# Kernel optimization log

Measured on AMD Instinct MI355X. Metric: run time of the kernel, lower is better.

Reference implementation:

```python
import jax, jax.numpy as jnp
import numpy as np
import math

B, N, DIM = 2, 2048, 1024
D_LAYERS, H, DH = 6, 8, 64
INNER = H * DH            # 512
FF_IN = int(DIM * 2 * 4 / 3)  # 2730 (GEGLU inner dim)
NB, MD = 32, 128          # rel-pos buckets / max distance
ALPHA = 0.1               # grad_shrink alpha
EPS = 1e-5


def setup_inputs() -> dict:
    key = jax.random.key(0)
    ks = jax.random.split(key, 8)
    s = 0.02
    return {
        "x": jax.random.normal(ks[0], (B, N, DIM), jnp.float32),
        "rel_emb": jax.random.normal(ks[1], (NB, H), jnp.float32) * s,
        "ln1_g": jnp.ones((D_LAYERS, DIM), jnp.float32),
        "ln1_b": jnp.zeros((D_LAYERS, DIM), jnp.float32),
        "wq": jax.random.normal(ks[2], (D_LAYERS, DIM, INNER), jnp.float32) * s,
        "wkv": jax.random.normal(ks[3], (D_LAYERS, DIM, 2 * DH), jnp.float32) * s,
        "wo": jax.random.normal(ks[4], (D_LAYERS, INNER, DIM), jnp.float32) * s,
        "ln2_g": jnp.ones((D_LAYERS, DIM), jnp.float32),
        "ln2_b": jnp.zeros((D_LAYERS, DIM), jnp.float32),
        "w1": jax.random.normal(ks[5], (D_LAYERS, DIM, 2 * FF_IN), jnp.float32) * s,
        "w2": jax.random.normal(ks[6], (D_LAYERS, FF_IN, DIM), jnp.float32) * s,
        "lnf_g": jnp.ones((DIM,), jnp.float32),
        "lnf_b": jnp.zeros((DIM,), jnp.float32),
    }


def _ln(x, g, b):
    mu = jnp.mean(x, axis=-1, keepdims=True)
    var = jnp.mean(jnp.square(x - mu), axis=-1, keepdims=True)
    return (x - mu) * jax.lax.rsqrt(var + EPS) * g + b


def _rel_pos_bias(rel_emb, n):
    pos = jnp.arange(n)
    rel = pos[None, :] - pos[:, None]        # k_pos - q_pos
    dist = jnp.maximum(-rel, 0)
    max_exact = NB // 2
    is_small = dist < max_exact
    val_large = max_exact + (
        jnp.log(jnp.maximum(dist, 1).astype(jnp.float32) / max_exact)
        / math.log(MD / max_exact) * (NB - max_exact)
    ).astype(jnp.int32)
    val_large = jnp.minimum(val_large, NB - 1)
    bucket = jnp.where(is_small, dist, val_large)
    return jnp.transpose(rel_emb[bucket], (2, 0, 1))  # [H, n, n]


def reference(x, rel_emb, ln1_g, ln1_b, wq, wkv, wo, ln2_g, ln2_b, w1, w2, lnf_g, lnf_b):
    b, n, _ = x.shape
    scale = DH ** -0.5
    # grad_shrink (forward identity, scales gradient by alpha)
    x = x * ALPHA + jax.lax.stop_gradient(x) * (1.0 - ALPHA)
    bias = _rel_pos_bias(rel_emb, n)               # [H, n, n]
    causal = jnp.triu(jnp.ones((n, n), bool), 1)   # mask above diagonal
    neg = -jnp.finfo(x.dtype).max
    for l in range(D_LAYERS):
        # --- causal self-attention (multi-query: shared k/v) ---
        xn = _ln(x, ln1_g[l], ln1_b[l])
        q = (xn @ wq[l]).reshape(b, n, H, DH).transpose(0, 2, 1, 3) * scale  # bhnd
        k, v = jnp.split(xn @ wkv[l], 2, axis=-1)                            # [b,n,DH] each
        sim = jnp.einsum('bhid,bjd->bhij', q, k) + bias[None]
        sim = jnp.where(causal, neg, sim)
        attn = jax.nn.softmax(sim, axis=-1)
        o = jnp.einsum('bhij,bjd->bhid', attn, v).transpose(0, 2, 1, 3).reshape(b, n, INNER)
        x = x + o @ wo[l]
        # --- GEGLU feedforward ---
        xn = _ln(x, ln2_g[l], ln2_b[l])
        h = xn @ w1[l]
        a, g = jnp.split(h, 2, axis=-1)
        x = x + (jax.nn.gelu(g, approximate=False) * a) @ w2[l]
    return _ln(x, lnf_g, lnf_b)
```

## Files before the change

kernel.cpp:

```cpp
#include <hip/hip_runtime.h>
#include <cstdint>
#include <cstddef>

using bf16 = __bf16;
typedef __bf16 bf16x8 __attribute__((ext_vector_type(8)));
typedef __bf16 bf16x4 __attribute__((ext_vector_type(4)));
typedef __bf16 bf16x2 __attribute__((ext_vector_type(2)));
typedef float  f32x4  __attribute__((ext_vector_type(4)));
typedef float  f32x16 __attribute__((ext_vector_type(16)));
typedef int    i32x4  __attribute__((ext_vector_type(4)));
typedef float  f32x4u __attribute__((ext_vector_type(4), aligned(4)));

constexpr int NB   = 2;
constexpr int NN   = 2048;
constexpr int DIM  = 1024;
constexpr int NH   = 8;
constexpr int DH   = 64;
constexpr int INNER= 512;
constexpr int QKVN = 640;
constexpr int FF   = 2730;
constexpr int FFP  = 2816;
constexpr int FF2N = 5632;
constexpr int MROW = NB * NN;
constexpr int NLAY = 6;
constexpr int AROWS = NB * NH * NN;
constexpr int NSPLIT = 4;

__device__ __forceinline__ void gload_lds16(const bf16* g, bf16* l) {
  __builtin_amdgcn_global_load_lds((const __attribute__((address_space(1))) void*)g,
                                   (__attribute__((address_space(3))) void*)l,
                                   16, 0, 0);
}

__device__ __forceinline__ int pack_bf16(float lo, float hi_) {
  bf16x2 t; t[0] = (bf16)lo; t[1] = (bf16)hi_;
  return __builtin_bit_cast(int, t);
}

__global__ void btab_kernel(const float* __restrict__ rel, float* __restrict__ btab) {
  int d = blockIdx.x * 256 + threadIdx.x;
  if (d >= NN) return;
  int bucket;
  if (d < 16) bucket = d;
  else {
    int vl = 16 + (int)(logf((float)d / 16.0f) / logf(8.0f) * 16.0f);
    bucket = vl < 31 ? vl : 31;
  }
  for (int h = 0; h < NH; ++h) btab[h * NN + d] = rel[bucket * NH + h];
}

__global__ void conv_tr(const float* __restrict__ src, size_t srcLayer, int srcStride,
                        int colOff, int R, int C,
                        bf16* __restrict__ dst, size_t dstLayer, int Tcols, float scale) {
  __shared__ float tile[32][33];
  const int i0 = blockIdx.x * 32, j0 = blockIdx.y * 32, z = blockIdx.z;
  const float* s = src + (size_t)z * srcLayer;
  bf16* d = dst + (size_t)z * dstLayer;
  const int tx = threadIdx.x, ty = threadIdx.y;
#pragma unroll
  for (int k = 0; k < 4; ++k) {
    int j = j0 + ty + k * 8;
    int i = i0 + tx;
    float v = 0.0f;
    if (j < R && i < C) v = s[(size_t)j * srcStride + colOff + i] * scale;
    tile[ty + k * 8][tx] = v;
  }
  __syncthreads();
#pragma unroll
  for (int k = 0; k < 4; ++k) {
    int i = i0 + ty + k * 8;
    int j = j0 + tx;
    d[(size_t)i * Tcols + j] = (bf16)tile[tx][ty + k * 8];
  }
}

template <typename OUT>
__global__ void ln_kernel(const float* __restrict__ X, const float* __restrict__ G,
                          const float* __restrict__ Bt, OUT* __restrict__ out) {
  __shared__ float red[8];
  const int row = blockIdx.x, t = threadIdx.x;
  const float* xr = X + (size_t)row * DIM;
  float4 v = *(const float4*)(xr + t * 4);
  float s  = v.x + v.y + v.z + v.w;
  float s2 = v.x * v.x + v.y * v.y + v.z * v.z + v.w * v.w;
#pragma unroll
  for (int o = 1; o < 64; o <<= 1) { s += __shfl_xor(s, o); s2 += __shfl_xor(s2, o); }
  if ((t & 63) == 0) { red[t >> 6] = s; red[4 + (t >> 6)] = s2; }
  __syncthreads();
  float S  = red[0] + red[1] + red[2] + red[3];
  float S2 = red[4] + red[5] + red[6] + red[7];
  const float inv = 1.0f / (float)DIM;
  float mu = S * inv;
  float var = S2 * inv - mu * mu;
  float rstd = rsqrtf(var + 1e-5f);
  float4 g  = *(const float4*)(G + t * 4);
  float4 bb = *(const float4*)(Bt + t * 4);
  OUT* orow = out + (size_t)row * DIM + t * 4;
  orow[0] = (OUT)((v.x - mu) * rstd * g.x + bb.x);
  orow[1] = (OUT)((v.y - mu) * rstd * g.y + bb.y);
  orow[2] = (OUT)((v.z - mu) * rstd * g.z + bb.z);
  orow[3] = (OUT)((v.w - mu) * rstd * g.w + bb.w);
}

template <int MODE>
__launch_bounds__(512)
__global__ void gemm_bt(const bf16* __restrict__ A, const bf16* __restrict__ B,
                        int K, int lda, int N, bf16* __restrict__ Cb, float* __restrict__ Xr) {
  __shared__ __align__(16) bf16 As[2][128 * 64];
  __shared__ __align__(16) bf16 Bs[2][128 * 64];
  const int tid = threadIdx.x;
  const int lane = tid & 63, wave = tid >> 6;
  const int gx = gridDim.x, gy = gridDim.y;
  const int nwg = gx * gy;
  const int orig = blockIdx.y * gx + blockIdx.x;
  const int wgid = (orig & 7) * (nwg >> 3) + (orig >> 3);
  const int m0 = (wgid % gy) * 128;
  const int n0 = (wgid / gy) * 128;
  const int wm = (wave >> 2) * 64, wn = (wave & 3) * 32;
  const int fr = lane & 15, fg8 = (lane >> 4) * 8;
  const int frl8 = (fr & 7) * 8;
  const int rL = lane >> 3;
  const int cS = ((lane & 7) ^ rL) * 8;
  const bf16* aB = A + (size_t)(m0 + wave * 8 + rL) * lda + cS;
  const bf16* bB = B + (size_t)(n0 + wave * 8 + rL) * K + cS;
  f32x4 acc[4][2] = {};

  auto STAGE = [&](int buf, int kt) {
#pragma unroll
    for (int r = 0; r < 2; ++r) {
      gload_lds16(aB + (size_t)(r * 64) * lda + kt, &As[buf][(r * 8 + wave) * 512]);
      gload_lds16(bB + (size_t)(r * 64) * K + kt, &Bs[buf][(r * 8 + wave) * 512]);
    }
  };

  STAGE(0, 0);
  const int nt = K >> 6;
  int cur = 0;
  for (int t = 0; t < nt; ++t) {
    asm volatile("s_waitcnt vmcnt(0)" ::: "memory");
    __builtin_amdgcn_s_barrier();
    __builtin_amdgcn_sched_barrier(0);
    if (t + 1 < nt) STAGE(cur ^ 1, (t + 1) * 64);
#pragma unroll
    for (int kk = 0; kk < 64; kk += 32) {
      bf16x8 af[4], bfr[2];
#pragma unroll
      for (int m = 0; m < 4; ++m)
        af[m] = *(const bf16x8*)&As[cur][(wm + m * 16 + fr) * 64 + ((kk + fg8) ^ frl8)];
#pragma unroll
      for (int n = 0; n < 2; ++n)
        bfr[n] = *(const bf16x8*)&Bs[cur][(wn + n * 16 + fr) * 64 + ((kk + fg8) ^ frl8)];
#pragma unroll
      for (int m = 0; m < 4; ++m)
#pragma unroll
        for (int n = 0; n < 2; ++n)
          acc[m][n] = __builtin_amdgcn_mfma_f32_16x16x32_bf16(af[m], bfr[n], acc[m][n], 0, 0, 0);
    }
    __builtin_amdgcn_sched_barrier(0);
    __builtin_amdgcn_s_barrier();
    cur ^= 1;
  }
  const int cc = lane & 15, cg = (lane >> 4) * 4;
#pragma unroll
  for (int m = 0; m < 4; ++m) {
#pragma unroll
    for (int n = 0; n < 2; ++n) {
      const int col = n0 + wn + n * 16 + cc;
#pragma unroll
      for (int r = 0; r < 4; ++r) {
        const int row = m0 + wm + m * 16 + cg + r;
        const size_t idx = (size_t)row * N + col;
        if (MODE == 0) Cb[idx] = (bf16)acc[m][n][r];
        else           Xr[idx] += acc[m][n][r];
      }
    }
  }
}

__global__ void vt_kernel(const bf16* __restrict__ QKV, bf16* __restrict__ VT) {
  __shared__ bf16 t[32][33];
  const int n0 = blockIdx.x * 32, d0 = blockIdx.y * 32, b = blockIdx.z;
  const int tx = threadIdx.x, ty = threadIdx.y;
#pragma unroll
  for (int k = 0; k < 4; ++k) {
    int n = n0 + ty + k * 8;
    t[ty + k * 8][tx] = QKV[(size_t)(b * NN + n) * QKVN + 576 + d0 + tx];
  }
  __syncthreads();
#pragma unroll
  for (int k = 0; k < 4; ++k) {
    int dh = d0 + ty + k * 8;
    VT[(size_t)(b * 64 + dh) * NN + n0 + tx] = t[tx][ty + k * 8];
  }
}

__launch_bounds__(256)
__global__ void attn_kernel(const bf16* __restrict__ QKV, const bf16* __restrict__ VT,
                            const float* __restrict__ btab,
                            float* __restrict__ Opart, float* __restrict__ mlbuf) {
  const int tid = threadIdx.x;
  const int lane = tid & 63, wv = tid >> 6;
  const int split = blockIdx.x & (NSPLIT - 1);
  const int qt = (NN / 32 - 1) - (blockIdx.x / NSPLIT);
  const int h = blockIdx.y * 4 + wv, b = blockIdx.z;
  const int q0 = qt * 32;
  const int qc = lane & 31;
  const int hid = lane >> 5;
  const int h8 = hid * 8;
  const int kv_full = q0 + 32;
  const int nt32 = kv_full >> 5;
  const int base = nt32 >> 2, rem = nt32 & 3;
  const int cnt = base + (split < rem ? 1 : 0);
  const int startT = split * base + (split < rem ? split : rem);
  const int lo = startT * 32;
  const int kend = lo + cnt * 32;
  const size_t obase = ((size_t)split * NB * NH + b * NH + h) * 64;
  const int Rbase = (b * NH + h) * NN + q0;
  if (cnt == 0) {
#pragma unroll
    for (int dd = 0; dd < 32; ++dd)
      Opart[(obase + dd * 2 + hid) * NN + q0 + qc] = 0.0f;
    if (hid == 0)
      ((float2*)mlbuf)[(size_t)split * AROWS + Rbase + qc] = make_float2(-1e30f, 0.0f);
    return;
  }
  const float* bt = btab + h * NN;
  bf16x8 qf[4];
#pragma unroll
  for (int ks = 0; ks < 4; ++ks)
    qf[ks] = *(const bf16x8*)&QKV[(size_t)(b * NN + q0 + qc) * QKVN + h * DH + ks * 16 + h8];

  f32x16 Oacc0 = {}, Oacc1 = {};
  float m_run = -1e30f, l_run = 0.0f;
  int kv0 = lo;

  while (kv0 < kend) {
    const bool interior = (kv0 + 32 <= q0);
    bf16x8 kf[4];
#pragma unroll
    for (int ks = 0; ks < 4; ++ks)
      kf[ks] = *(const bf16x8*)&QKV[(size_t)(b * NN + kv0 + qc) * QKVN + 512 + ks * 16 + h8];
    bf16x8 vf[2][2];
#pragma unroll
    for (int dblk = 0; dblk < 2; ++dblk)
#pragma unroll
      for (int ks2 = 0; ks2 < 2; ++ks2)
        vf[dblk][ks2] = *(const bf16x8*)&VT[(size_t)(b * 64 + dblk * 32 + qc) * NN + kv0 + ks2 * 16 + h8];
    __builtin_amdgcn_s_setprio(1);
    f32x16 S = {};
#pragma unroll
    for (int ks = 0; ks < 4; ++ks)
      S = __builtin_amdgcn_mfma_f32_32x32x16_bf16(kf[ks], qf[ks], S, 0, 0, 0);
    __builtin_amdgcn_s_setprio(0);
    float sv[16];
    float mx = -1e30f;
    if (interior) {
      f32x4 bv[4];
#pragma unroll
      for (int g = 0; g < 4; ++g)
        bv[g] = *(const f32x4u*)(bt + (q0 + qc - kv0 - 8 * g - 4 * hid - 3));
#pragma unroll
      for (int g = 0; g < 4; ++g)
#pragma unroll
        for (int e = 0; e < 4; ++e) {
          const float val = S[g * 4 + e] + bv[g][3 - e];
          sv[g * 4 + e] = val;
          mx = fmaxf(mx, val);
        }
    } else {
#pragma unroll
      for (int r = 0; r < 16; ++r) {
        const int kvr = (r & 3) + 8 * (r >> 2) + 4 * hid;
        const int d = (q0 + qc) - (kv0 + kvr);
        const int dc = d > 0 ? d : 0;
        float val = S[r] + bt[dc];
        if (d < 0) val = -1e30f;
        sv[r] = val;
        mx = fmaxf(mx, val);
      }
    }
    if (!__all(mx <= m_run + 8.0f)) {
      mx = fmaxf(mx, __shfl_xor(mx, 32));
      const float m_new = fmaxf(m_run, mx);
      const float sc = __expf(m_run - m_new);
      l_run *= sc;
#pragma unroll
      for (int r = 0; r < 16; ++r) { Oacc0[r] *= sc; Oacc1[r] *= sc; }
      m_run = m_new;
    }
    float csum = 0.0f;
#pragma unroll
    for (int r = 0; r < 16; ++r) { sv[r] = __expf(sv[r] - m_run); csum += sv[r]; }
    csum += __shfl_xor(csum, 32);
    l_run += csum;
    int w[8];
#pragma unroll
    for (int g = 0; g < 4; ++g) {
      w[2 * g]     = pack_bf16(sv[4 * g],     sv[4 * g + 1]);
      w[2 * g + 1] = pack_bf16(sv[4 * g + 2], sv[4 * g + 3]);
    }
    bf16x8 pfrag[2];
#pragma unroll
    for (int ks2 = 0; ks2 < 2; ++ks2) {
      const int a  = w[4 * ks2],     bb = w[4 * ks2 + 1];
      const int c  = w[4 * ks2 + 2], dd = w[4 * ks2 + 3];
      const int s0 = hid ? a : c,    s1 = hid ? bb : dd;
      const int r0 = __shfl_xor(s0, 32);
      const int r1 = __shfl_xor(s1, 32);
      i32x4 fw;
      fw[0] = hid ? r0 : a;
      fw[1] = hid ? r1 : bb;
      fw[2] = hid ? c  : r0;
      fw[3] = hid ? dd : r1;
      pfrag[ks2] = __builtin_bit_cast(bf16x8, fw);
    }
    __builtin_amdgcn_s_setprio(1);
#pragma unroll
    for (int ks2 = 0; ks2 < 2; ++ks2) {
      Oacc0 = __builtin_amdgcn_mfma_f32_32x32x16_bf16(vf[0][ks2], pfrag[ks2], Oacc0, 0, 0, 0);
      Oacc1 = __builtin_amdgcn_mfma_f32_32x32x16_bf16(vf[1][ks2], pfrag[ks2], Oacc1, 0, 0, 0);
    }
    __builtin_amdgcn_s_setprio(0);
    kv0 += 32;
  }
#pragma unroll
  for (int r = 0; r < 16; ++r) {
    const int dl = (r & 3) + 8 * (r >> 2) + 4 * hid;
    Opart[(obase + dl) * NN + q0 + qc]      = Oacc0[r];
    Opart[(obase + 32 + dl) * NN + q0 + qc] = Oacc1[r];
  }
  if (hid == 0)
    ((float2*)mlbuf)[(size_t)split * AROWS + Rbase + qc] = make_float2(m_run, l_run);
}

__global__ void attn_combine(const float* __restrict__ Opart, const float* __restrict__ mlbuf,
                             bf16* __restrict__ O) {
  const int gtid = blockIdx.x * 256 + threadIdx.x;
  const int q  = gtid & (NN - 1);
  const int dq = (gtid >> 11) & 15;
  const int bh = gtid >> 15;
  const int R = bh * NN + q;
  float2 ml[NSPLIT];
  float m = -1e30f;
#pragma unroll
  for (int s = 0; s < NSPLIT; ++s) {
    ml[s] = ((const float2*)mlbuf)[(size_t)s * AROWS + R];
    m = fmaxf(m, ml[s].x);
  }
  float w[NSPLIT];
  float denom = 0.0f;
#pragma unroll
  for (int s = 0; s < NSPLIT; ++s) {
    w[s] = __expf(ml[s].x - m);
    denom += ml[s].y * w[s];
  }
  const float inv = 1.0f / denom;
  float o[4] = {};
#pragma unroll
  for (int s = 0; s < NSPLIT; ++s) {
    const size_t rbase = ((size_t)(s * NB * NH + bh) * 64 + dq * 4) * NN + q;
#pragma unroll
    for (int j = 0; j < 4; ++j) o[j] += Opart[rbase + j * NN] * w[s];
  }
  bf16x4 res;
#pragma unroll
  for (int j = 0; j < 4; ++j) res[j] = (bf16)(o[j] * inv);
  const int h = bh & (NH - 1), b = bh >> 3;
  *(bf16x4*)&O[(size_t)(b * NN + q) * INNER + h * DH + dq * 4] = res;
}

__global__ void gelu_mul_kernel(bf16* __restrict__ h) {
  const size_t total = (size_t)MROW * FFP / 8;
  for (size_t i = (size_t)blockIdx.x * blockDim.x + threadIdx.x; i < total;
       i += (size_t)gridDim.x * blockDim.x) {
    const size_t row = i / (FFP / 8), c8 = i % (FFP / 8);
    bf16* base = h + row * FF2N + c8 * 8;
    bf16x8 a = *(const bf16x8*)base;
    bf16x8 g = *(const bf16x8*)(base + FFP);
    bf16x8 r;
#pragma unroll
    for (int j = 0; j < 8; ++j) {
      float gv = (float)g[j], av = (float)a[j];
      float ge = 0.5f * gv * (1.0f + erff(gv * 0.70710678118654752f));
      r[j] = (bf16)(ge * av);
    }
    *(bf16x8*)base = r;
  }
}

extern "C" void kernel_launch(void* const* d_in, const int* in_sizes, int n_in,
                              void* d_out, int out_size, void* d_ws, size_t ws_size,
                              hipStream_t stream) {
  (void)in_sizes; (void)n_in; (void)out_size;
  const float* in_x  = (const float*)d_in[0];
  const float* rel   = (const float*)d_in[1];
  const float* ln1g  = (const float*)d_in[2];
  const float* ln1b  = (const float*)d_in[3];
  const float* wq    = (const float*)d_in[4];
  const float* wkv   = (const float*)d_in[5];
  const float* wo    = (const float*)d_in[6];
  const float* ln2g  = (const float*)d_in[7];
  const float* ln2b  = (const float*)d_in[8];
  const float* w1    = (const float*)d_in[9];
  const float* w2    = (const float*)d_in[10];
  const float* lnfg  = (const float*)d_in[11];
  const float* lnfb  = (const float*)d_in[12];
  float* out = (float*)d_out;

  constexpr size_t E_QKV = (size_t)QKVN * DIM;
  constexpr size_t E_WO  = (size_t)DIM * INNER;
  constexpr size_t E_W1F = (size_t)FF2N * DIM;
  constexpr size_t E_W2  = (size_t)DIM * FFP;
  bf16* wqkvT = (bf16*)d_ws;
  bf16* woT  = wqkvT + NLAY * E_QKV;
  bf16* w1fT = woT  + NLAY * E_WO;
  bf16* w2T  = w1fT + NLAY * E_W1F;
  bf16* xnb  = w2T  + NLAY * E_W2;
  bf16* qkvb = xnb  + (size_t)MROW * DIM;
  bf16* vTb  = qkvb + (size_t)MROW * QKVN;
  bf16* ob   = vTb  + (size_t)NB * 64 * NN;
  bf16* hb   = ob   + (size_t)MROW * INNER;
  float* xbuf = (float*)(hb + (size_t)MROW * FF2N);
  float* btab = xbuf + (size_t)MROW * DIM;
  const size_t needed = (size_t)((char*)(btab + NH * NN) - (char*)d_ws);
  if (ws_size < needed) return;
  float* Opart = (float*)hb;
  float* mlbuf = (float*)(hb + (size_t)18 * 1024 * 1024);
  hipMemcpyAsync(xbuf, in_x, (size_t)MROW * DIM * sizeof(float),
                 hipMemcpyDeviceToDevice, stream);
  btab_kernel<<<8, 256, 0, stream>>>(rel, btab);

  const dim3 tb(32, 8);
  conv_tr<<<dim3(16, 32, 6), tb, 0, stream>>>(wq,  (size_t)DIM*INNER, INNER, 0, DIM, INNER,
                                              wqkvT, E_QKV, DIM, 0.125f);
  conv_tr<<<dim3(4, 32, 6),  tb, 0, stream>>>(wkv, (size_t)DIM*128, 128, 0, DIM, 128,
                                              wqkvT + (size_t)INNER*DIM, E_QKV, DIM, 1.0f);
  conv_tr<<<dim3(32, 16, 6), tb, 0, stream>>>(wo,  (size_t)INNER*DIM, DIM, 0, INNER, DIM,
                                              woT,  E_WO, INNER, 1.0f);
  conv_tr<<<dim3(88, 32, 6), tb, 0, stream>>>(w1,  (size_t)DIM*2*FF, 2*FF, 0, DIM, FF,
                                              w1fT, E_W1F, DIM, 1.0f);
  conv_tr<<<dim3(88, 32, 6), tb, 0, stream>>>(w1,  (size_t)DIM*2*FF, 2*FF, FF, DIM, FF,
                                              w1fT + (size_t)FFP*DIM, E_W1F, DIM, 1.0f);
  conv_tr<<<dim3(32, 88, 6), tb, 0, stream>>>(w2,  (size_t)FF*DIM, DIM, 0, FF, DIM,
                                              w2T,  E_W2, FFP, 1.0f);

  for (int l = 0; l < NLAY; ++l) {
    ln_kernel<bf16><<<MROW, 256, 0, stream>>>(xbuf, ln1g + l*DIM, ln1b + l*DIM, xnb);
    gemm_bt<0><<<dim3(QKVN/128, MROW/128), 512, 0, stream>>>(xnb, wqkvT + l*E_QKV, DIM, DIM, QKVN, qkvb, nullptr);
    vt_kernel<<<dim3(NN/32, 2, NB), tb, 0, stream>>>(qkvb, vTb);
    attn_kernel<<<dim3((NN/32)*NSPLIT, NH/4, NB), 256, 0, stream>>>(qkvb, vTb, btab, Opart, mlbuf);
    attn_combine<<<AROWS*16/256, 256, 0, stream>>>(Opart, mlbuf, ob);
    gemm_bt<1><<<dim3(DIM/128, MROW/128), 512, 0, stream>>>(ob, woT + l*E_WO, INNER, INNER, DIM, nullptr, xbuf);
    ln_kernel<bf16><<<MROW, 256, 0, stream>>>(xbuf, ln2g + l*DIM, ln2b + l*DIM, xnb);
    gemm_bt<0><<<dim3(FF2N/128, MROW/128), 512, 0, stream>>>(xnb, w1fT + l*E_W1F, DIM, DIM, FF2N, hb, nullptr);
    gelu_mul_kernel<<<2048, 256, 0, stream>>>(hb);
    gemm_bt<1><<<dim3(DIM/128, MROW/128), 512, 0, stream>>>(hb, w2T + l*E_W2, FFP, FF2N, DIM, nullptr, xbuf);
  }
  ln_kernel<float><<<MROW, 256, 0, stream>>>(xbuf, lnfg, lnfb, out);
}
```

Baseline: 1.740 ms.

## Fuse GEGLU into W1 GEMM epilogue via interleaved weights; row-major attention partials

The value and gate halves of W1 are interleaved in blocks of 16 rows so that each warp's two N-fragments hold matching a/g columns. The GEMM epilogue then applies erf-GELU and the multiply directly and writes a compact FFP-wide activation. This removes the separate gelu_mul pass and halves the hidden-activation write and read traffic. Separately, the attention partial outputs are stored row-major per query (64 contiguous floats) so the combine kernel can do vectorized float4 loads instead of strided scalar ones.

Measured after the change: 1.668 ms. 1.04x faster.

```diff
diff --git a/kernel.cpp b/kernel.cpp
--- a/kernel.cpp
+++ b/kernel.cpp
@@ -51,7 +51,8 @@
 
 __global__ void conv_tr(const float* __restrict__ src, size_t srcLayer, int srcStride,
                         int colOff, int R, int C,
-                        bf16* __restrict__ dst, size_t dstLayer, int Tcols, float scale) {
+                        bf16* __restrict__ dst, size_t dstLayer, int Tcols, float scale,
+                        int rowOff16) {
   __shared__ float tile[32][33];
   const int i0 = blockIdx.x * 32, j0 = blockIdx.y * 32, z = blockIdx.z;
   const float* s = src + (size_t)z * srcLayer;
@@ -70,7 +71,8 @@
   for (int k = 0; k < 4; ++k) {
     int i = i0 + ty + k * 8;
     int j = j0 + tx;
-    d[(size_t)i * Tcols + j] = (bf16)tile[tx][ty + k * 8];
+    int dr = (rowOff16 >= 0) ? (((i >> 4) << 5) + rowOff16 + (i & 15)) : i;
+    d[(size_t)dr * Tcols + j] = (bf16)tile[tx][ty + k * 8];
   }
 }
 
@@ -161,17 +163,31 @@
     cur ^= 1;
   }
   const int cc = lane & 15, cg = (lane >> 4) * 4;
-#pragma unroll
-  for (int m = 0; m < 4; ++m) {
-#pragma unroll
-    for (int n = 0; n < 2; ++n) {
-      const int col = n0 + wn + n * 16 + cc;
+  if (MODE == 2) {
+    const int jcol = (n0 + wn) / 2 + cc;
+#pragma unroll
+    for (int m = 0; m < 4; ++m) {
 #pragma unroll
       for (int r = 0; r < 4; ++r) {
         const int row = m0 + wm + m * 16 + cg + r;
-        const size_t idx = (size_t)row * N + col;
-        if (MODE == 0) Cb[idx] = (bf16)acc[m][n][r];
-        else           Xr[idx] += acc[m][n][r];
+        const float av = acc[m][0][r], gv = acc[m][1][r];
+        const float ge = 0.5f * gv * (1.0f + erff(gv * 0.70710678118654752f)) * av;
+        Cb[(size_t)row * N + jcol] = (bf16)ge;
+      }
+    }
+  } else {
+#pragma unroll
+    for (int m = 0; m < 4; ++m) {
+#pragma unroll
+      for (int n = 0; n < 2; ++n) {
+        const int col = n0 + wn + n * 16 + cc;
+#pragma unroll
+        for (int r = 0; r < 4; ++r) {
+          const int row = m0 + wm + m * 16 + cg + r;
+          const size_t idx = (size_t)row * N + col;
+          if (MODE == 0) Cb[idx] = (bf16)acc[m][n][r];
+          else           Xr[idx] += acc[m][n][r];
+        }
       }
     }
   }
@@ -214,12 +230,12 @@
   const int startT = split * base + (split < rem ? split : rem);
   const int lo = startT * 32;
   const int kend = lo + cnt * 32;
-  const size_t obase = ((size_t)split * NB * NH + b * NH + h) * 64;
+  const size_t obase = ((size_t)(split * NB * NH) + b * NH + h) * NN;
   const int Rbase = (b * NH + h) * NN + q0;
+  float* prow = Opart + (obase + q0 + qc) * 64;
   if (cnt == 0) {
 #pragma unroll
-    for (int dd = 0; dd < 32; ++dd)
-      Opart[(obase + dd * 2 + hid) * NN + q0 + qc] = 0.0f;
+    for (int dd = 0; dd < 32; ++dd) prow[dd * 2 + hid] = 0.0f;
     if (hid == 0)
       ((float2*)mlbuf)[(size_t)split * AROWS + Rbase + qc] = make_float2(-1e30f, 0.0f);
     return;
@@ -326,8 +342,8 @@
 #pragma unroll
   for (int r = 0; r < 16; ++r) {
     const int dl = (r & 3) + 8 * (r >> 2) + 4 * hid;
-    Opart[(obase + dl) * NN + q0 + qc]      = Oacc0[r];
-    Opart[(obase + 32 + dl) * NN + q0 + qc] = Oacc1[r];
+    prow[dl]      = Oacc0[r];
+    prow[32 + dl] = Oacc1[r];
   }
   if (hid == 0)
     ((float2*)mlbuf)[(size_t)split * AROWS + Rbase + qc] = make_float2(m_run, l_run);
@@ -336,8 +352,8 @@
 __global__ void attn_combine(const float* __restrict__ Opart, const float* __restrict__ mlbuf,
                              bf16* __restrict__ O) {
   const int gtid = blockIdx.x * 256 + threadIdx.x;
-  const int q  = gtid & (NN - 1);
-  const int dq = (gtid >> 11) & 15;
+  const int dq = gtid & 15;
+  const int q  = (gtid >> 4) & (NN - 1);
   const int bh = gtid >> 15;
   const int R = bh * NN + q;
   float2 ml[NSPLIT];
@@ -358,34 +374,15 @@
   float o[4] = {};
 #pragma unroll
   for (int s = 0; s < NSPLIT; ++s) {
-    const size_t rbase = ((size_t)(s * NB * NH + bh) * 64 + dq * 4) * NN + q;
-#pragma unroll
-    for (int j = 0; j < 4; ++j) o[j] += Opart[rbase + j * NN] * w[s];
+    const f32x4 v = *(const f32x4*)(Opart + ((size_t)(s * NB * NH + bh) * NN + q) * 64 + dq * 4);
+#pragma unroll
+    for (int j = 0; j < 4; ++j) o[j] += v[j] * w[s];
   }
   bf16x4 res;
 #pragma unroll
   for (int j = 0; j < 4; ++j) res[j] = (bf16)(o[j] * inv);
   const int h = bh & (NH - 1), b = bh >> 3;
   *(bf16x4*)&O[(size_t)(b * NN + q) * INNER + h * DH + dq * 4] = res;
-}
-
-__global__ void gelu_mul_kernel(bf16* __restrict__ h) {
-  const size_t total = (size_t)MROW * FFP / 8;
-  for (size_t i = (size_t)blockIdx.x * blockDim.x + threadIdx.x; i < total;
-       i += (size_t)gridDim.x * blockDim.x) {
-    const size_t row = i / (FFP / 8), c8 = i % (FFP / 8);
-    bf16* base = h + row * FF2N + c8 * 8;
-    bf16x8 a = *(const bf16x8*)base;
-    bf16x8 g = *(const bf16x8*)(base + FFP);
-    bf16x8 r;
-#pragma unroll
-    for (int j = 0; j < 8; ++j) {
-      float gv = (float)g[j], av = (float)a[j];
-      float ge = 0.5f * gv * (1.0f + erff(gv * 0.70710678118654752f));
-      r[j] = (bf16)(ge * av);
-    }
-    *(bf16x8*)base = r;
-  }
 }
 
 extern "C" void kernel_launch(void* const* d_in, const int* in_sizes, int n_in,
@@ -432,17 +429,17 @@
 
   const dim3 tb(32, 8);
   conv_tr<<<dim3(16, 32, 6), tb, 0, stream>>>(wq,  (size_t)DIM*INNER, INNER, 0, DIM, INNER,
-                                              wqkvT, E_QKV, DIM, 0.125f);
+                                              wqkvT, E_QKV, DIM, 0.125f, -1);
   conv_tr<<<dim3(4, 32, 6),  tb, 0, stream>>>(wkv, (size_t)DIM*128, 128, 0, DIM, 128,
-                                              wqkvT + (size_t)INNER*DIM, E_QKV, DIM, 1.0f);
+                                              wqkvT + (size_t)INNER*DIM, E_QKV, DIM, 1.0f, -1);
   conv_tr<<<dim3(32, 16, 6), tb, 0, stream>>>(wo,  (size_t)INNER*DIM, DIM, 0, INNER, DIM,
-                                              woT,  E_WO, INNER, 1.0f);
+                                              woT,  E_WO, INNER, 1.0f, -1);
   conv_tr<<<dim3(88, 32, 6), tb, 0, stream>>>(w1,  (size_t)DIM*2*FF, 2*FF, 0, DIM, FF,
-                                              w1fT, E_W1F, DIM, 1.0f);
+                                              w1fT, E_W1F, DIM, 1.0f, 0);
   conv_tr<<<dim3(88, 32, 6), tb, 0, stream>>>(w1,  (size_t)DIM*2*FF, 2*FF, FF, DIM, FF,
-                                              w1fT + (size_t)FFP*DIM, E_W1F, DIM, 1.0f);
+                                              w1fT, E_W1F, DIM, 1.0f, 16);
   conv_tr<<<dim3(32, 88, 6), tb, 0, stream>>>(w2,  (size_t)FF*DIM, DIM, 0, FF, DIM,
-                                              w2T,  E_W2, FFP, 1.0f);
+                                              w2T,  E_W2, FFP, 1.0f, -1);
 
   for (int l = 0; l < NLAY; ++l) {
     ln_kernel<bf16><<<MROW, 256, 0, stream>>>(xbuf, ln1g + l*DIM, ln1b + l*DIM, xnb);
@@ -452,9 +449,8 @@
     attn_combine<<<AROWS*16/256, 256, 0, stream>>>(Opart, mlbuf, ob);
     gemm_bt<1><<<dim3(DIM/128, MROW/128), 512, 0, stream>>>(ob, woT + l*E_WO, INNER, INNER, DIM, nullptr, xbuf);
     ln_kernel<bf16><<<MROW, 256, 0, stream>>>(xbuf, ln2g + l*DIM, ln2b + l*DIM, xnb);
-    gemm_bt<0><<<dim3(FF2N/128, MROW/128), 512, 0, stream>>>(xnb, w1fT + l*E_W1F, DIM, DIM, FF2N, hb, nullptr);
-    gelu_mul_kernel<<<2048, 256, 0, stream>>>(hb);
-    gemm_bt<1><<<dim3(DIM/128, MROW/128), 512, 0, stream>>>(hb, w2T + l*E_W2, FFP, FF2N, DIM, nullptr, xbuf);
+    gemm_bt<2><<<dim3(FF2N/128, MROW/128), 512, 0, stream>>>(xnb, w1fT + l*E_W1F, DIM, DIM, FFP, hb, nullptr);
+    gemm_bt<1><<<dim3(DIM/128, MROW/128), 512, 0, stream>>>(hb, w2T + l*E_W2, FFP, FFP, DIM, nullptr, xbuf);
   }
   ln_kernel<float><<<MROW, 256, 0, stream>>>(xbuf, lnfg, lnfb, out);
 }
```
